# Kernel optimization log

Hardware: AMD Instinct MI355X
Metric: run time of the kernel (lower is better)

The kernel has to match this reference:

```python
import jax, jax.numpy as jnp
import numpy as np

N_STOCKS = 65536
HIDDEN = 512
N_INDUSTRIES = 128
NEG_SLOPE = 0.01  # nn.LeakyReLU default


def setup_inputs() -> dict:
    key = jax.random.key(0)
    k1, k2, k3 = jax.random.split(key, 3)
    e_s = jax.random.normal(k1, (N_STOCKS, HIDDEN), dtype=jnp.float32)
    # one industry per stock -> exactly N_STOCKS ones in the incidence matrix
    ind = jax.random.randint(k2, (N_STOCKS,), 0, N_INDUSTRIES)
    industry_matrix = jax.nn.one_hot(ind, N_INDUSTRIES, dtype=jnp.int32)
    # HypergraphConv params: lin (no bias) + output bias
    weight = jax.random.normal(k3, (HIDDEN, HIDDEN), dtype=jnp.float32) / np.sqrt(HIDDEN)
    bias = jnp.zeros((HIDDEN,), dtype=jnp.float32)
    return {"e_s": e_s, "industry_matrix": industry_matrix, "weight": weight, "bias": bias}


def reference(e_s, industry_matrix, weight, bias):
    N, H = e_s.shape
    E = industry_matrix.shape[1]
    # torch.where(industry_matrix == 1): static size N (one-hot rows)
    stock_idx, ind_idx = jnp.nonzero(industry_matrix == 1, size=N)
    x = e_s @ weight  # lin projection
    ones = jnp.ones((N,), dtype=e_s.dtype)
    # node degree D (hyperedge_weight defaults to 1) and edge degree B
    D = jax.ops.segment_sum(ones, stock_idx, num_segments=N)
    Dinv = jnp.where(D > 0, 1.0 / D, 0.0)
    B = jax.ops.segment_sum(ones, ind_idx, num_segments=E)
    Binv = jnp.where(B > 0, 1.0 / B, 0.0)
    # node -> hyperedge: B^{-1} H^T X Theta
    edge_feat = jax.ops.segment_sum(x[stock_idx], ind_idx, num_segments=E) * Binv[:, None]
    # hyperedge -> node: D^{-1} H (edge_feat)
    out = jax.ops.segment_sum(edge_feat[ind_idx], stock_idx, num_segments=N) * Dinv[:, None]
    out = out + bias
    # LeakyReLU
    return jnp.where(out >= 0, out, NEG_SLOPE * out)
```

## Files before the change

### kernel.cpp

```cpp
#include <hip/hip_runtime.h>

#define NS 65536
#define HID 512
#define NE 128
#define NEG 0.01f

typedef int   vi4 __attribute__((ext_vector_type(4)));
typedef float vf4 __attribute__((ext_vector_type(4)));

__global__ __launch_bounds__(1024) void k_find(const int* __restrict__ im,
                                               int* __restrict__ ind) {
    __shared__ int lind[256];
    const int b = blockIdx.x, t = threadIdx.x;
    const vi4* p = reinterpret_cast<const vi4*>(im) + (size_t)b * 8192;
#pragma unroll
    for (int j = t; j < 8192; j += 1024) {
        vi4 v = __builtin_nontemporal_load(p + j);
        int s = j >> 5;
        int c = (j & 31) << 2;
        if (v[0] == 1) lind[s] = c;
        if (v[1] == 1) lind[s] = c + 1;
        if (v[2] == 1) lind[s] = c + 2;
        if (v[3] == 1) lind[s] = c + 3;
    }
    __syncthreads();
    if (t < 256) ind[b * 256 + t] = lind[t];
}

__global__ __launch_bounds__(1024) void k_agg(const float* __restrict__ e_s,
                                              const int* __restrict__ ind,
                                              float* __restrict__ partial,
                                              int* __restrict__ counts) {
    __shared__ int rows[1024];
    __shared__ vf4 red[1024];
    __shared__ int cntL;
    const int e = blockIdx.x >> 2;
    const int q = blockIdx.x & 3;
    const int t = threadIdx.x;
    if (t == 0) cntL = 0;
    __syncthreads();
    const int base = q * (NS / 4);
#pragma unroll
    for (int k = 0; k < (NS / 4) / 1024; ++k) {
        int idx = base + k * 1024 + t;
        if (ind[idx] == e) {
            int p = atomicAdd(&cntL, 1);
            if (p < 1024) rows[p] = idx;
        }
    }
    __syncthreads();
    const int cnt = (cntL < 1024) ? cntL : 1024;
    const int g = t >> 7;
    const int l = t & 127;
    vf4 acc = {0.f, 0.f, 0.f, 0.f};
#pragma unroll 4
    for (int i = g; i < cnt; i += 8) {
        int row = rows[i];
        vf4 v = __builtin_nontemporal_load(
            reinterpret_cast<const vf4*>(e_s + (size_t)row * HID) + l);
        acc += v;
    }
    red[t] = acc;
    __syncthreads();
    if (g == 0) {
        vf4 a = red[l];
#pragma unroll
        for (int p = 1; p < 8; ++p) a += red[l + p * 128];
        reinterpret_cast<vf4*>(partial + ((size_t)(q * NE + e)) * HID)[l] = a;
    }
    if (t == 0) counts[q * NE + e] = cnt;
}

__global__ __launch_bounds__(1024) void k_gemm_out(const float* __restrict__ partial,
                                                   const float* __restrict__ W,
                                                   const float* __restrict__ bias,
                                                   const int* __restrict__ ind,
                                                   const int* __restrict__ counts,
                                                   float* __restrict__ out) {
    __shared__ float aL[HID];
    __shared__ float redf[1024];
    __shared__ float rowL[HID];
    __shared__ int rows[1024];
    __shared__ int cntL;
    const int e = blockIdx.x >> 1;
    const int h = blockIdx.x & 1;
    const int t = threadIdx.x;
    if (t == 0) cntL = 0;
    if (t < HID) {
        float s = 0.f;
#pragma unroll
        for (int q = 0; q < 4; ++q) s += partial[((size_t)(q * NE + e)) * HID + t];
        aL[t] = s;
    }
    __syncthreads();

    const int base = h * (NS / 2);
#pragma unroll
    for (int k = 0; k < (NS / 2) / 1024; ++k) {
        int idx = base + k * 1024 + t;
        if (ind[idx] == e) {
            int p = atomicAdd(&cntL, 1);
            if (p < 1024) rows[p] = idx;
        }
    }

    const int j  = t & (HID - 1);
    const int hh = t >> 9;
    const int k0 = hh * 256;
    float acc = 0.f;
#pragma unroll 8
    for (int k = k0; k < k0 + 256; ++k)
        acc += aL[k] * W[k * HID + j];
    redf[t] = acc;
    __syncthreads();
    if (t < HID) {
        int tot = counts[e] + counts[NE + e] + counts[2 * NE + e] + counts[3 * NE + e];
        float binv = (tot > 0) ? 1.0f / (float)tot : 0.0f;
        float v = (redf[t] + redf[t + HID]) * binv + bias[t];
        rowL[t] = (v >= 0.0f) ? v : NEG * v;
    }
    __syncthreads();

    const int cnt = (cntL < 1024) ? cntL : 1024;
    const int g = t >> 7;
    const int l = t & 127;
    const vf4 r4 = reinterpret_cast<const vf4*>(rowL)[l];
#pragma unroll 2
    for (int i = g; i < cnt; i += 8) {
        int s = rows[i];
        __builtin_nontemporal_store(r4, reinterpret_cast<vf4*>(out + (size_t)s * HID) + l);
    }
}

extern "C" void kernel_launch(void* const* d_in, const int* in_sizes, int n_in,
                              void* d_out, int out_size, void* d_ws, size_t ws_size,
                              hipStream_t stream) {
    const float* e_s  = (const float*)d_in[0];
    const int*   im   = (const int*)d_in[1];
    const float* W    = (const float*)d_in[2];
    const float* bias = (const float*)d_in[3];
    float* out = (float*)d_out;

    char* ws = (char*)d_ws;
    int*   ind     = (int*)(ws + 0);
    float* partial = (float*)(ws + 262144);
    int*   counts  = (int*)(ws + 1310720);

    k_find    <<<256, 1024, 0, stream>>>(im, ind);
    k_agg     <<<NE * 4, 1024, 0, stream>>>(e_s, ind, partial, counts);
    k_gemm_out<<<NE * 2, 1024, 0, stream>>>(partial, W, bias, ind, counts, out);
}
```

Measured before the change: 80.86 us.

## Split edge GEMM from output write and gather edge rows per stock

```diff
diff --git a/kernel.cpp b/kernel.cpp
--- a/kernel.cpp
+++ b/kernel.cpp
@@ -71,21 +71,15 @@
     if (t == 0) counts[q * NE + e] = cnt;
 }
 
-__global__ __launch_bounds__(1024) void k_gemm_out(const float* __restrict__ partial,
-                                                   const float* __restrict__ W,
-                                                   const float* __restrict__ bias,
-                                                   const int* __restrict__ ind,
-                                                   const int* __restrict__ counts,
-                                                   float* __restrict__ out) {
+__global__ __launch_bounds__(1024) void k_gemm(const float* __restrict__ partial,
+                                               const float* __restrict__ W,
+                                               const float* __restrict__ bias,
+                                               const int* __restrict__ counts,
+                                               float* __restrict__ efrow) {
     __shared__ float aL[HID];
     __shared__ float redf[1024];
-    __shared__ float rowL[HID];
-    __shared__ int rows[1024];
-    __shared__ int cntL;
-    const int e = blockIdx.x >> 1;
-    const int h = blockIdx.x & 1;
+    const int e = blockIdx.x;
     const int t = threadIdx.x;
-    if (t == 0) cntL = 0;
     if (t < HID) {
         float s = 0.f;
 #pragma unroll
@@ -93,17 +87,6 @@
         aL[t] = s;
     }
     __syncthreads();
-
-    const int base = h * (NS / 2);
-#pragma unroll
-    for (int k = 0; k < (NS / 2) / 1024; ++k) {
-        int idx = base + k * 1024 + t;
-        if (ind[idx] == e) {
-            int p = atomicAdd(&cntL, 1);
-            if (p < 1024) rows[p] = idx;
-        }
-    }
-
     const int j  = t & (HID - 1);
     const int hh = t >> 9;
     const int k0 = hh * 256;
@@ -117,18 +100,25 @@
         int tot = counts[e] + counts[NE + e] + counts[2 * NE + e] + counts[3 * NE + e];
         float binv = (tot > 0) ? 1.0f / (float)tot : 0.0f;
         float v = (redf[t] + redf[t + HID]) * binv + bias[t];
-        rowL[t] = (v >= 0.0f) ? v : NEG * v;
+        efrow[(size_t)e * HID + t] = (v >= 0.0f) ? v : NEG * v;
     }
+}
+
+__global__ __launch_bounds__(1024) void k_out(const float* __restrict__ efrow,
+                                              const int* __restrict__ ind,
+                                              float* __restrict__ out) {
+    __shared__ int lindL[256];
+    const int b = blockIdx.x, t = threadIdx.x;
+    if (t < 256) lindL[t] = ind[b * 256 + t];
     __syncthreads();
-
-    const int cnt = (cntL < 1024) ? cntL : 1024;
     const int g = t >> 7;
     const int l = t & 127;
-    const vf4 r4 = reinterpret_cast<const vf4*>(rowL)[l];
-#pragma unroll 2
-    for (int i = g; i < cnt; i += 8) {
-        int s = rows[i];
-        __builtin_nontemporal_store(r4, reinterpret_cast<vf4*>(out + (size_t)s * HID) + l);
+    vf4* outp = reinterpret_cast<vf4*>(out) + (size_t)b * 256 * 128;
+#pragma unroll 4
+    for (int ls = g; ls < 256; ls += 8) {
+        int e = lindL[ls];
+        vf4 v = reinterpret_cast<const vf4*>(efrow + (size_t)e * HID)[l];
+        __builtin_nontemporal_store(v, outp + ls * 128 + l);
     }
 }
 
@@ -144,9 +134,11 @@
     char* ws = (char*)d_ws;
     int*   ind     = (int*)(ws + 0);
     float* partial = (float*)(ws + 262144);
+    float* efrow   = (float*)(ws + 262144);
     int*   counts  = (int*)(ws + 1310720);
 
-    k_find    <<<256, 1024, 0, stream>>>(im, ind);
-    k_agg     <<<NE * 4, 1024, 0, stream>>>(e_s, ind, partial, counts);
-    k_gemm_out<<<NE * 2, 1024, 0, stream>>>(partial, W, bias, ind, counts, out);
+    k_find<<<256, 1024, 0, stream>>>(im, ind);
+    k_agg <<<NE * 4, 1024, 0, stream>>>(e_s, ind, partial, counts);
+    k_gemm<<<NE, 1024, 0, stream>>>(partial, W, bias, counts, efrow);
+    k_out <<<256, 1024, 0, stream>>>(efrow, ind, out);
 }
```

Measured after the change: 76.95 us. 4.8% less time.
